# Kernel optimization log

Hardware: AMD Instinct MI355X
Metric: run time of the kernel (lower is better)

## Reference

```python
import jax, jax.numpy as jnp
import numpy as np

N_NODES = 100000
N_EDGES = 1200000
EMBED_DIM = 64
N_LAYERS = 3


def setup_inputs() -> dict:
    key = jax.random.key(0)
    k1, k2, k3, k4 = jax.random.split(key, 4)
    embeddings = jax.random.normal(k1, (N_NODES, EMBED_DIM), dtype=jnp.float32)
    edge_weight = jax.random.uniform(k2, (N_EDGES,), dtype=jnp.float32)
    edge_src = jax.random.randint(k3, (N_EDGES,), 0, N_NODES, dtype=jnp.int32)
    edge_dst = jax.random.randint(k4, (N_EDGES,), 0, N_NODES, dtype=jnp.int32)
    return {"embeddings": embeddings, "edge_weight": edge_weight,
            "edge_src": edge_src, "edge_dst": edge_dst}


def _spmm(edge_src, edge_dst, edge_weight, x):
    # (A @ x)[d] = sum_{e: dst(e)=d} w[e] * x[src(e)]  -- COO SpMM via gather + segment_sum
    msgs = edge_weight[:, None] * x[edge_src]  # [E, D]
    return jax.ops.segment_sum(msgs, edge_dst, num_segments=N_NODES)


def reference(embeddings, edge_weight, edge_src, edge_dst):
    all_embeddings = [embeddings]
    ego = embeddings
    for _ in range(N_LAYERS):
        ego = _spmm(edge_src, edge_dst, edge_weight, ego)
        all_embeddings.append(ego)
    # stack layer outputs: [n_layers+1, N, D]
    return jnp.stack(all_embeddings, axis=0)
```

## Files before the change

### kernel.cpp

```cpp
#include <hip/hip_runtime.h>


#define N_NODES 100000
#define DIM 64
#define SCAN_CHUNK 1024

#define NR 8
#define RSIZE ((N_NODES + NR - 1) / NR)
#define SLICES 256

typedef int   vint4   __attribute__((ext_vector_type(4)));
typedef float vfloat4 __attribute__((ext_vector_type(4)));

__device__ __forceinline__ int xcd_id() {
    int x;
    asm volatile("s_getreg_b32 %0, hwreg(HW_REG_XCC_ID)" : "=s"(x));
    return x & (NR - 1);
}


__global__ void hist_kernel(const int* __restrict__ edst, int* __restrict__ deg, int E) {
    int i = blockIdx.x * blockDim.x + threadIdx.x;
    int nv = E >> 2;
    if (i < nv) {
        vint4 d = __builtin_nontemporal_load(((const vint4*)edst) + i);
        atomicAdd(&deg[d[0]], 1);
        atomicAdd(&deg[d[1]], 1);
        atomicAdd(&deg[d[2]], 1);
        atomicAdd(&deg[d[3]], 1);
    }
    if (i == 0) {
        for (int e = nv << 2; e < E; ++e) atomicAdd(&deg[edst[e]], 1);
    }
}

__global__ void scan1_kernel(const int* __restrict__ deg, int* __restrict__ off,
                             int* __restrict__ bsum, int n) {
    __shared__ int sdata[256];
    int tid = threadIdx.x;
    int base = blockIdx.x * SCAN_CHUNK + tid * 4;
    int v[4];
    #pragma unroll
    for (int i = 0; i < 4; ++i) v[i] = (base + i < n) ? deg[base + i] : 0;
    int tsum = v[0] + v[1] + v[2] + v[3];
    sdata[tid] = tsum;
    __syncthreads();
    for (int d = 1; d < 256; d <<= 1) {
        int t = (tid >= d) ? sdata[tid - d] : 0;
        __syncthreads();
        sdata[tid] += t;
        __syncthreads();
    }
    int excl = sdata[tid] - tsum;
    if (tid == 255) bsum[blockIdx.x] = sdata[255];
    int run = excl;
    #pragma unroll
    for (int i = 0; i < 4; ++i) {
        if (base + i < n) off[base + i] = run;
        run += v[i];
    }
}

__global__ void scan2_kernel(int* __restrict__ bsum, int nb) {
    __shared__ int s[128];
    int tid = threadIdx.x;
    int v = (tid < nb) ? bsum[tid] : 0;
    s[tid] = v;
    __syncthreads();
    for (int d = 1; d < 128; d <<= 1) {
        int t = (tid >= d) ? s[tid - d] : 0;
        __syncthreads();
        s[tid] += t;
        __syncthreads();
    }
    if (tid < nb) bsum[tid] = s[tid] - v;
}

__global__ void scan3_kernel(int* __restrict__ off, int* __restrict__ cur,
                             const int* __restrict__ bsum, int n) {
    int i = blockIdx.x * blockDim.x + threadIdx.x;
    if (i < n) {
        int v = off[i] + bsum[i / SCAN_CHUNK];
        off[i] = v;
        cur[i] = v;
    }
}

__global__ void scatter_xcd_kernel(const int* __restrict__ esrc, const int* __restrict__ edst,
                                   const float* __restrict__ ew, int* __restrict__ cur,
                                   int2* __restrict__ pairs, int* __restrict__ ticket,
                                   int E, int chunk) {
    const int r = xcd_id();
    const int lo = r * RSIZE;
    const int hi = min(lo + RSIZE, N_NODES);
    __shared__ int s_sl;
    for (;;) {
        if (threadIdx.x == 0) s_sl = atomicAdd(&ticket[r], 1);
        __syncthreads();
        const int s = s_sl;
        __syncthreads();
        if (s >= SLICES) return;
        const int e0 = s * chunk;
        if (e0 >= E) continue;
        const int e1 = min(e0 + chunk, E);
        const int nv = (e1 - e0) >> 2;
        const vint4*   s4 = (const vint4*)(esrc + e0);
        const vint4*   d4 = (const vint4*)(edst + e0);
        const vfloat4* w4 = (const vfloat4*)(ew + e0);
        for (int i = threadIdx.x; i < nv; i += blockDim.x) {
            vint4 dd = __builtin_nontemporal_load(d4 + i);
            vint4 ss = __builtin_nontemporal_load(s4 + i);
            vfloat4 ww = __builtin_nontemporal_load(w4 + i);
            #pragma unroll
            for (int j = 0; j < 4; ++j) {
                int dj = dd[j];
                if (dj >= lo && dj < hi) {
                    int p = atomicAdd(&cur[dj], 1);
                    int2 pr;
                    pr.x = ss[j];
                    pr.y = __float_as_int(ww[j]);
                    pairs[p] = pr;
                }
            }
        }
        for (int e = e0 + (nv << 2) + threadIdx.x; e < e1; e += blockDim.x) {
            int dj = edst[e];
            if (dj >= lo && dj < hi) {
                int p = atomicAdd(&cur[dj], 1);
                int2 pr;
                pr.x = esrc[e];
                pr.y = __float_as_int(ew[e]);
                pairs[p] = pr;
            }
        }
    }
}


__global__ void spmm_csr_kernel(const float* __restrict__ x,
                                const int2* __restrict__ pairs,
                                const int* __restrict__ off,
                                const int* __restrict__ deg,
                                float* __restrict__ y) {
    int gtid = blockIdx.x * blockDim.x + threadIdx.x;
    int node = gtid >> 6;
    int lane = threadIdx.x & 63;
    int o  = lane >> 3;
    int ol = lane & 7;
    if (node >= N_NODES) return;
    int s0 = off[node];
    int n  = deg[node];
    float4 a0 = make_float4(0.f, 0.f, 0.f, 0.f);
    float4 a1 = make_float4(0.f, 0.f, 0.f, 0.f);
    for (int k = o; k < n; k += 8) {
        int2 pr = pairs[s0 + k];
        float w = __int_as_float(pr.y);
        const float4* row = (const float4*)(x + (size_t)pr.x * DIM);
        float4 v0 = row[ol];
        float4 v1 = row[ol + 8];
        a0.x += w * v0.x; a0.y += w * v0.y; a0.z += w * v0.z; a0.w += w * v0.w;
        a1.x += w * v1.x; a1.y += w * v1.y; a1.z += w * v1.z; a1.w += w * v1.w;
    }
    #pragma unroll
    for (int d = 8; d <= 32; d <<= 1) {
        a0.x += __shfl_xor(a0.x, d); a0.y += __shfl_xor(a0.y, d);
        a0.z += __shfl_xor(a0.z, d); a0.w += __shfl_xor(a0.w, d);
        a1.x += __shfl_xor(a1.x, d); a1.y += __shfl_xor(a1.y, d);
        a1.z += __shfl_xor(a1.z, d); a1.w += __shfl_xor(a1.w, d);
    }
    if (o == 0) {
        vfloat4* yrow = (vfloat4*)(y + (size_t)node * DIM);
        vfloat4 r0 = { a0.x, a0.y, a0.z, a0.w };
        vfloat4 r1 = { a1.x, a1.y, a1.z, a1.w };
        __builtin_nontemporal_store(r0, yrow + ol);
        __builtin_nontemporal_store(r1, yrow + ol + 8);
    }
}


__global__ void spmm_atomic_kernel(const float* __restrict__ x, const float* __restrict__ ew,
                                   const int* __restrict__ esrc, const int* __restrict__ edst,
                                   float* __restrict__ y, int n_edges) {
    long long tid = (long long)blockIdx.x * blockDim.x + threadIdx.x;
    int e = (int)(tid >> 6);
    int d = (int)(tid & 63);
    if (e >= n_edges) return;
    int s = esrc[e]; int t = edst[e]; float w = ew[e];
    atomicAdd(&y[(long long)t * DIM + d], w * x[(long long)s * DIM + d]);
}

extern "C" void kernel_launch(void* const* d_in, const int* in_sizes, int n_in,
                              void* d_out, int out_size, void* d_ws, size_t ws_size,
                              hipStream_t stream) {
    const float* emb  = (const float*)d_in[0];
    const float* ew   = (const float*)d_in[1];
    const int*   esrc = (const int*)d_in[2];
    const int*   edst = (const int*)d_in[3];
    float* out = (float*)d_out;

    const int E = in_sizes[1];
    const size_t layer_elems = (size_t)N_NODES * DIM;

    size_t need = (size_t)E * 8 + (size_t)3 * N_NODES * 4 + 1024;
    hipMemcpyAsync(out, emb, layer_elems * sizeof(float), hipMemcpyDeviceToDevice, stream);

    if (ws_size >= need) {
        char* w = (char*)d_ws;
        int2* pairs = (int2*)w;
        int* deg    = (int*)(w + (size_t)E * 8);
        int* cur    = deg + N_NODES;
        int* off    = cur + N_NODES;
        int* bsum   = off + N_NODES;
        int* ticket = bsum + 128;

        hipMemsetAsync(deg, 0, (size_t)N_NODES * 4, stream);
        hipMemsetAsync(ticket, 0, NR * 4, stream);

        const int nv4 = E >> 2;
        hist_kernel<<<(nv4 + 255) / 256, 256, 0, stream>>>(edst, deg, E);

        const int nscan = (N_NODES + SCAN_CHUNK - 1) / SCAN_CHUNK;
        scan1_kernel<<<nscan, 256, 0, stream>>>(deg, off, bsum, N_NODES);
        scan2_kernel<<<1, 128, 0, stream>>>(bsum, nscan);
        scan3_kernel<<<(N_NODES + 255) / 256, 256, 0, stream>>>(off, cur, bsum, N_NODES);

        const int chunk = (((E + SLICES - 1) / SLICES) + 3) & ~3;
        scatter_xcd_kernel<<<1024, 256, 0, stream>>>(esrc, edst, ew, cur, pairs, ticket, E, chunk);

        const int nb = (N_NODES + 3) / 4;
        for (int l = 1; l <= 3; ++l) {
            spmm_csr_kernel<<<nb, 256, 0, stream>>>(
                out + (size_t)(l - 1) * layer_elems, pairs, off, deg,
                out + (size_t)l * layer_elems);
        }
    } else {
        hipMemsetAsync(out + layer_elems, 0, 3 * layer_elems * sizeof(float), stream);
        const long long total_threads = (long long)E * 64;
        const int blocks = (int)((total_threads + 255) / 256);
        for (int l = 1; l <= 3; ++l) {
            spmm_atomic_kernel<<<blocks, 256, 0, stream>>>(
                out + (size_t)(l - 1) * layer_elems, ew, esrc, edst,
                out + (size_t)l * layer_elems, E);
        }
    }
}
```

Measured before the change: 405.6 us.

## Simplify scatter to flat kernel and widen per-edge row gather in CSR SpMM

Drops the XCD-partitioned ticket-based scatter, which made each of the 8 XCD groups re-read the whole edge list, in favour of a single flat pass with global atomics on the cursor array. The SpMM kernel now gives each edge 4 lanes, each loading 4 float4 chunks, so 16 edges are in flight per wavefront instead of 8. Each wavefront preloads the first 64 (src, weight) pairs cooperatively and broadcasts them with shuffles, falling back to direct loads beyond 64 neighbours. The trade-off is that scatter atomics and pair writes lose the per-XCD L2 locality the old scheme aimed for, and the reduction needs more shuffles.

```diff
diff --git a/kernel.cpp b/kernel.cpp
--- a/kernel.cpp
+++ b/kernel.cpp
@@ -5,18 +5,8 @@
 #define DIM 64
 #define SCAN_CHUNK 1024
 
-#define NR 8
-#define RSIZE ((N_NODES + NR - 1) / NR)
-#define SLICES 256
-
 typedef int   vint4   __attribute__((ext_vector_type(4)));
 typedef float vfloat4 __attribute__((ext_vector_type(4)));
-
-__device__ __forceinline__ int xcd_id() {
-    int x;
-    asm volatile("s_getreg_b32 %0, hwreg(HW_REG_XCC_ID)" : "=s"(x));
-    return x & (NR - 1);
-}
 
 
 __global__ void hist_kernel(const int* __restrict__ edst, int* __restrict__ deg, int E) {
@@ -86,52 +76,31 @@
     }
 }
 
-__global__ void scatter_xcd_kernel(const int* __restrict__ esrc, const int* __restrict__ edst,
-                                   const float* __restrict__ ew, int* __restrict__ cur,
-                                   int2* __restrict__ pairs, int* __restrict__ ticket,
-                                   int E, int chunk) {
-    const int r = xcd_id();
-    const int lo = r * RSIZE;
-    const int hi = min(lo + RSIZE, N_NODES);
-    __shared__ int s_sl;
-    for (;;) {
-        if (threadIdx.x == 0) s_sl = atomicAdd(&ticket[r], 1);
-        __syncthreads();
-        const int s = s_sl;
-        __syncthreads();
-        if (s >= SLICES) return;
-        const int e0 = s * chunk;
-        if (e0 >= E) continue;
-        const int e1 = min(e0 + chunk, E);
-        const int nv = (e1 - e0) >> 2;
-        const vint4*   s4 = (const vint4*)(esrc + e0);
-        const vint4*   d4 = (const vint4*)(edst + e0);
-        const vfloat4* w4 = (const vfloat4*)(ew + e0);
-        for (int i = threadIdx.x; i < nv; i += blockDim.x) {
-            vint4 dd = __builtin_nontemporal_load(d4 + i);
-            vint4 ss = __builtin_nontemporal_load(s4 + i);
-            vfloat4 ww = __builtin_nontemporal_load(w4 + i);
-            #pragma unroll
-            for (int j = 0; j < 4; ++j) {
-                int dj = dd[j];
-                if (dj >= lo && dj < hi) {
-                    int p = atomicAdd(&cur[dj], 1);
-                    int2 pr;
-                    pr.x = ss[j];
-                    pr.y = __float_as_int(ww[j]);
-                    pairs[p] = pr;
-                }
-            }
-        }
-        for (int e = e0 + (nv << 2) + threadIdx.x; e < e1; e += blockDim.x) {
-            int dj = edst[e];
-            if (dj >= lo && dj < hi) {
-                int p = atomicAdd(&cur[dj], 1);
-                int2 pr;
-                pr.x = esrc[e];
-                pr.y = __float_as_int(ew[e]);
-                pairs[p] = pr;
-            }
+__global__ void scatter_kernel(const int* __restrict__ esrc, const int* __restrict__ edst,
+                               const float* __restrict__ ew, int* __restrict__ cur,
+                               int2* __restrict__ pairs, int E) {
+    int i = blockIdx.x * blockDim.x + threadIdx.x;
+    int nv = E >> 2;
+    if (i < nv) {
+        vint4 dd = __builtin_nontemporal_load(((const vint4*)edst) + i);
+        vint4 ss = __builtin_nontemporal_load(((const vint4*)esrc) + i);
+        vfloat4 ww = __builtin_nontemporal_load(((const vfloat4*)ew) + i);
+        #pragma unroll
+        for (int j = 0; j < 4; ++j) {
+            int p = atomicAdd(&cur[dd[j]], 1);
+            int2 pr;
+            pr.x = ss[j];
+            pr.y = __float_as_int(ww[j]);
+            pairs[p] = pr;
+        }
+    }
+    if (i == 0) {
+        for (int e = nv << 2; e < E; ++e) {
+            int p = atomicAdd(&cur[edst[e]], 1);
+            int2 pr;
+            pr.x = esrc[e];
+            pr.y = __float_as_int(ew[e]);
+            pairs[p] = pr;
         }
     }
 }
@@ -145,35 +114,62 @@
     int gtid = blockIdx.x * blockDim.x + threadIdx.x;
     int node = gtid >> 6;
     int lane = threadIdx.x & 63;
-    int o  = lane >> 3;
-    int ol = lane & 7;
+    int g  = lane >> 2;
+    int gl = lane & 3;
     if (node >= N_NODES) return;
     int s0 = off[node];
     int n  = deg[node];
+
+    int2 pr0; pr0.x = 0; pr0.y = 0;
+    if (lane < n) pr0 = pairs[s0 + lane];
+
     float4 a0 = make_float4(0.f, 0.f, 0.f, 0.f);
-    float4 a1 = make_float4(0.f, 0.f, 0.f, 0.f);
-    for (int k = o; k < n; k += 8) {
-        int2 pr = pairs[s0 + k];
-        float w = __int_as_float(pr.y);
-        const float4* row = (const float4*)(x + (size_t)pr.x * DIM);
-        float4 v0 = row[ol];
-        float4 v1 = row[ol + 8];
-        a0.x += w * v0.x; a0.y += w * v0.y; a0.z += w * v0.z; a0.w += w * v0.w;
-        a1.x += w * v1.x; a1.y += w * v1.y; a1.z += w * v1.z; a1.w += w * v1.w;
+    float4 a1 = a0, a2 = a0, a3 = a0;
+
+    int trips = (n + 15) >> 4;
+    for (int t = 0; t < trips; ++t) {
+        int k = g + (t << 4);
+        int idx = min(k, 63);
+        int src = __shfl(pr0.x, idx);
+        int wb  = __shfl(pr0.y, idx);
+        if (k >= 64 && k < n) {
+            int2 p2 = pairs[s0 + k];
+            src = p2.x; wb = p2.y;
+        }
+        if (k < n) {
+            float w = __int_as_float(wb);
+            const float4* row = (const float4*)(x + (size_t)src * DIM);
+            float4 v0 = row[gl];
+            float4 v1 = row[gl + 4];
+            float4 v2 = row[gl + 8];
+            float4 v3 = row[gl + 12];
+            a0.x += w * v0.x; a0.y += w * v0.y; a0.z += w * v0.z; a0.w += w * v0.w;
+            a1.x += w * v1.x; a1.y += w * v1.y; a1.z += w * v1.z; a1.w += w * v1.w;
+            a2.x += w * v2.x; a2.y += w * v2.y; a2.z += w * v2.z; a2.w += w * v2.w;
+            a3.x += w * v3.x; a3.y += w * v3.y; a3.z += w * v3.z; a3.w += w * v3.w;
+        }
     }
     #pragma unroll
-    for (int d = 8; d <= 32; d <<= 1) {
+    for (int d = 4; d <= 32; d <<= 1) {
         a0.x += __shfl_xor(a0.x, d); a0.y += __shfl_xor(a0.y, d);
         a0.z += __shfl_xor(a0.z, d); a0.w += __shfl_xor(a0.w, d);
         a1.x += __shfl_xor(a1.x, d); a1.y += __shfl_xor(a1.y, d);
         a1.z += __shfl_xor(a1.z, d); a1.w += __shfl_xor(a1.w, d);
-    }
-    if (o == 0) {
+        a2.x += __shfl_xor(a2.x, d); a2.y += __shfl_xor(a2.y, d);
+        a2.z += __shfl_xor(a2.z, d); a2.w += __shfl_xor(a2.w, d);
+        a3.x += __shfl_xor(a3.x, d); a3.y += __shfl_xor(a3.y, d);
+        a3.z += __shfl_xor(a3.z, d); a3.w += __shfl_xor(a3.w, d);
+    }
+    if (g == 0) {
         vfloat4* yrow = (vfloat4*)(y + (size_t)node * DIM);
         vfloat4 r0 = { a0.x, a0.y, a0.z, a0.w };
         vfloat4 r1 = { a1.x, a1.y, a1.z, a1.w };
-        __builtin_nontemporal_store(r0, yrow + ol);
-        __builtin_nontemporal_store(r1, yrow + ol + 8);
+        vfloat4 r2 = { a2.x, a2.y, a2.z, a2.w };
+        vfloat4 r3 = { a3.x, a3.y, a3.z, a3.w };
+        __builtin_nontemporal_store(r0, yrow + gl);
+        __builtin_nontemporal_store(r1, yrow + gl + 4);
+        __builtin_nontemporal_store(r2, yrow + gl + 8);
+        __builtin_nontemporal_store(r3, yrow + gl + 12);
     }
 }
 
@@ -211,21 +207,19 @@
         int* cur    = deg + N_NODES;
         int* off    = cur + N_NODES;
         int* bsum   = off + N_NODES;
-        int* ticket = bsum + 128;
 
         hipMemsetAsync(deg, 0, (size_t)N_NODES * 4, stream);
-        hipMemsetAsync(ticket, 0, NR * 4, stream);
 
         const int nv4 = E >> 2;
-        hist_kernel<<<(nv4 + 255) / 256, 256, 0, stream>>>(edst, deg, E);
+        const int vb = (nv4 + 255) / 256;
+        hist_kernel<<<vb, 256, 0, stream>>>(edst, deg, E);
 
         const int nscan = (N_NODES + SCAN_CHUNK - 1) / SCAN_CHUNK;
         scan1_kernel<<<nscan, 256, 0, stream>>>(deg, off, bsum, N_NODES);
         scan2_kernel<<<1, 128, 0, stream>>>(bsum, nscan);
         scan3_kernel<<<(N_NODES + 255) / 256, 256, 0, stream>>>(off, cur, bsum, N_NODES);
 
-        const int chunk = (((E + SLICES - 1) / SLICES) + 3) & ~3;
-        scatter_xcd_kernel<<<1024, 256, 0, stream>>>(esrc, edst, ew, cur, pairs, ticket, E, chunk);
+        scatter_kernel<<<vb, 256, 0, stream>>>(esrc, edst, ew, cur, pairs, E);
 
         const int nb = (N_NODES + 3) / 4;
         for (int l = 1; l <= 3; ++l) {
```

Result: slower. 482.5 us (+19.0%).

## Gather fp16 copies of layer embeddings in SpMM and drop XCD ticket scatter

Applied to the files above, without the earlier changes.

Adds a conversion kernel that copies the input embeddings to the output and writes an fp16 shadow copy. Each SpMM layer now gathers neighbor rows from fp16 buffers, halving gather bytes, and writes both fp32 output and an fp16 copy for the next layer. The scatter kernel replaces the XCD-id ticket-based dynamic slicing with a static blockIdx-based range split using fewer slices. Feeding fp16-rounded values into later layers adds accumulated precision error relative to the fp32 reference.

```diff
diff --git a/kernel.cpp b/kernel.cpp
--- a/kernel.cpp
+++ b/kernel.cpp
@@ -1,4 +1,5 @@
 #include <hip/hip_runtime.h>
+#include <hip/hip_fp16.h>
 
 
 #define N_NODES 100000
@@ -7,15 +8,30 @@
 
 #define NR 8
 #define RSIZE ((N_NODES + NR - 1) / NR)
-#define SLICES 256
+#define SLICES 128
 
 typedef int   vint4   __attribute__((ext_vector_type(4)));
 typedef float vfloat4 __attribute__((ext_vector_type(4)));
 
-__device__ __forceinline__ int xcd_id() {
-    int x;
-    asm volatile("s_getreg_b32 %0, hwreg(HW_REG_XCC_ID)" : "=s"(x));
-    return x & (NR - 1);
+union HU { unsigned u; __half2 h; };
+
+__global__ void convert_kernel(const float* __restrict__ emb, float* __restrict__ out0,
+                               unsigned short* __restrict__ xh0, int n8) {
+    int i = blockIdx.x * blockDim.x + threadIdx.x;
+    if (i >= n8) return;
+    const vfloat4* e4 = (const vfloat4*)emb;
+    vfloat4 a = __builtin_nontemporal_load(e4 + 2 * i);
+    vfloat4 b = __builtin_nontemporal_load(e4 + 2 * i + 1);
+    vfloat4* o4 = (vfloat4*)out0;
+    __builtin_nontemporal_store(a, o4 + 2 * i);
+    __builtin_nontemporal_store(b, o4 + 2 * i + 1);
+    HU c0, c1, c2, c3;
+    c0.h = __float22half2_rn(make_float2(a[0], a[1]));
+    c1.h = __float22half2_rn(make_float2(a[2], a[3]));
+    c2.h = __float22half2_rn(make_float2(b[0], b[1]));
+    c3.h = __float22half2_rn(make_float2(b[2], b[3]));
+    vint4 p = { (int)c0.u, (int)c1.u, (int)c2.u, (int)c3.u };
+    ((vint4*)xh0)[i] = p;
 }
 
 
@@ -86,53 +102,96 @@
     }
 }
 
-__global__ void scatter_xcd_kernel(const int* __restrict__ esrc, const int* __restrict__ edst,
-                                   const float* __restrict__ ew, int* __restrict__ cur,
-                                   int2* __restrict__ pairs, int* __restrict__ ticket,
-                                   int E, int chunk) {
-    const int r = xcd_id();
+__global__ void scatter_range_kernel(const int* __restrict__ esrc, const int* __restrict__ edst,
+                                     const float* __restrict__ ew, int* __restrict__ cur,
+                                     int2* __restrict__ pairs, int E, int chunk) {
+    const int r = blockIdx.x & (NR - 1);
+    const int s = blockIdx.x / NR;
     const int lo = r * RSIZE;
     const int hi = min(lo + RSIZE, N_NODES);
-    __shared__ int s_sl;
-    for (;;) {
-        if (threadIdx.x == 0) s_sl = atomicAdd(&ticket[r], 1);
-        __syncthreads();
-        const int s = s_sl;
-        __syncthreads();
-        if (s >= SLICES) return;
-        const int e0 = s * chunk;
-        if (e0 >= E) continue;
-        const int e1 = min(e0 + chunk, E);
-        const int nv = (e1 - e0) >> 2;
-        const vint4*   s4 = (const vint4*)(esrc + e0);
-        const vint4*   d4 = (const vint4*)(edst + e0);
-        const vfloat4* w4 = (const vfloat4*)(ew + e0);
-        for (int i = threadIdx.x; i < nv; i += blockDim.x) {
-            vint4 dd = __builtin_nontemporal_load(d4 + i);
-            vint4 ss = __builtin_nontemporal_load(s4 + i);
-            vfloat4 ww = __builtin_nontemporal_load(w4 + i);
-            #pragma unroll
-            for (int j = 0; j < 4; ++j) {
-                int dj = dd[j];
-                if (dj >= lo && dj < hi) {
-                    int p = atomicAdd(&cur[dj], 1);
-                    int2 pr;
-                    pr.x = ss[j];
-                    pr.y = __float_as_int(ww[j]);
-                    pairs[p] = pr;
-                }
-            }
-        }
-        for (int e = e0 + (nv << 2) + threadIdx.x; e < e1; e += blockDim.x) {
-            int dj = edst[e];
+    const int e0 = s * chunk;
+    if (e0 >= E) return;
+    const int e1 = min(e0 + chunk, E);
+    const int nv = (e1 - e0) >> 2;
+    const vint4*   s4 = (const vint4*)(esrc + e0);
+    const vint4*   d4 = (const vint4*)(edst + e0);
+    const vfloat4* w4 = (const vfloat4*)(ew + e0);
+    for (int i = threadIdx.x; i < nv; i += blockDim.x) {
+        vint4 dd = __builtin_nontemporal_load(d4 + i);
+        vint4 ss = __builtin_nontemporal_load(s4 + i);
+        vfloat4 ww = __builtin_nontemporal_load(w4 + i);
+        #pragma unroll
+        for (int j = 0; j < 4; ++j) {
+            int dj = dd[j];
             if (dj >= lo && dj < hi) {
                 int p = atomicAdd(&cur[dj], 1);
                 int2 pr;
-                pr.x = esrc[e];
-                pr.y = __float_as_int(ew[e]);
+                pr.x = ss[j];
+                pr.y = __float_as_int(ww[j]);
                 pairs[p] = pr;
             }
         }
+    }
+    for (int e = e0 + (nv << 2) + threadIdx.x; e < e1; e += blockDim.x) {
+        int dj = edst[e];
+        if (dj >= lo && dj < hi) {
+            int p = atomicAdd(&cur[dj], 1);
+            int2 pr;
+            pr.x = esrc[e];
+            pr.y = __float_as_int(ew[e]);
+            pairs[p] = pr;
+        }
+    }
+}
+
+
+__global__ void spmm_h_kernel(const unsigned short* __restrict__ xh,
+                              const int2* __restrict__ pairs,
+                              const int* __restrict__ off,
+                              const int* __restrict__ deg,
+                              float* __restrict__ y,
+                              unsigned short* __restrict__ yh) {
+    int gtid = blockIdx.x * blockDim.x + threadIdx.x;
+    int node = gtid >> 6;
+    int lane = threadIdx.x & 63;
+    int o  = lane >> 3;
+    int ol = lane & 7;
+    if (node >= N_NODES) return;
+    int s0 = off[node];
+    int n  = deg[node];
+    float a0 = 0.f, a1 = 0.f, a2 = 0.f, a3 = 0.f;
+    float a4 = 0.f, a5 = 0.f, a6 = 0.f, a7 = 0.f;
+    for (int k = o; k < n; k += 8) {
+        int2 pr = pairs[s0 + k];
+        float w = __int_as_float(pr.y);
+        const vint4* row = (const vint4*)(xh + (size_t)pr.x * DIM);
+        vint4 v = row[ol];
+        HU c; float2 f;
+        c.u = (unsigned)v[0]; f = __half22float2(c.h); a0 += w * f.x; a1 += w * f.y;
+        c.u = (unsigned)v[1]; f = __half22float2(c.h); a2 += w * f.x; a3 += w * f.y;
+        c.u = (unsigned)v[2]; f = __half22float2(c.h); a4 += w * f.x; a5 += w * f.y;
+        c.u = (unsigned)v[3]; f = __half22float2(c.h); a6 += w * f.x; a7 += w * f.y;
+    }
+    #pragma unroll
+    for (int d = 8; d <= 32; d <<= 1) {
+        a0 += __shfl_xor(a0, d); a1 += __shfl_xor(a1, d);
+        a2 += __shfl_xor(a2, d); a3 += __shfl_xor(a3, d);
+        a4 += __shfl_xor(a4, d); a5 += __shfl_xor(a5, d);
+        a6 += __shfl_xor(a6, d); a7 += __shfl_xor(a7, d);
+    }
+    if (o == 0) {
+        float* yr = y + (size_t)node * DIM + ol * 8;
+        vfloat4 r0 = { a0, a1, a2, a3 };
+        vfloat4 r1 = { a4, a5, a6, a7 };
+        __builtin_nontemporal_store(r0, (vfloat4*)yr);
+        __builtin_nontemporal_store(r1, (vfloat4*)yr + 1);
+        HU c0, c1, c2, c3;
+        c0.h = __float22half2_rn(make_float2(a0, a1));
+        c1.h = __float22half2_rn(make_float2(a2, a3));
+        c2.h = __float22half2_rn(make_float2(a4, a5));
+        c3.h = __float22half2_rn(make_float2(a6, a7));
+        vint4 p = { (int)c0.u, (int)c1.u, (int)c2.u, (int)c3.u };
+        *((vint4*)(yh + (size_t)node * DIM + ol * 8)) = p;
     }
 }
 
@@ -151,7 +210,7 @@
     int s0 = off[node];
     int n  = deg[node];
     float4 a0 = make_float4(0.f, 0.f, 0.f, 0.f);
-    float4 a1 = make_float4(0.f, 0.f, 0.f, 0.f);
+    float4 a1 = a0;
     for (int k = o; k < n; k += 8) {
         int2 pr = pairs[s0 + k];
         float w = __int_as_float(pr.y);
@@ -201,20 +260,23 @@
     const int E = in_sizes[1];
     const size_t layer_elems = (size_t)N_NODES * DIM;
 
-    size_t need = (size_t)E * 8 + (size_t)3 * N_NODES * 4 + 1024;
-    hipMemcpyAsync(out, emb, layer_elems * sizeof(float), hipMemcpyDeviceToDevice, stream);
-
-    if (ws_size >= need) {
+    const size_t need_h   = (size_t)E * 8 + 2 * layer_elems * 2 + (size_t)3 * N_NODES * 4 + 1024;
+    const size_t need_f32 = (size_t)E * 8 + (size_t)3 * N_NODES * 4 + 1024;
+
+    if (ws_size >= need_h && E >= 4) {
         char* w = (char*)d_ws;
         int2* pairs = (int2*)w;
-        int* deg    = (int*)(w + (size_t)E * 8);
-        int* cur    = deg + N_NODES;
-        int* off    = cur + N_NODES;
-        int* bsum   = off + N_NODES;
-        int* ticket = bsum + 128;
+        unsigned short* xh0 = (unsigned short*)(w + (size_t)E * 8);
+        unsigned short* xh1 = xh0 + layer_elems;
+        int* deg  = (int*)(xh1 + layer_elems);
+        int* cur  = deg + N_NODES;
+        int* off  = cur + N_NODES;
+        int* bsum = off + N_NODES;
 
         hipMemsetAsync(deg, 0, (size_t)N_NODES * 4, stream);
-        hipMemsetAsync(ticket, 0, NR * 4, stream);
+
+        const int n8 = (int)(layer_elems / 8);
+        convert_kernel<<<(n8 + 255) / 256, 256, 0, stream>>>(emb, out, xh0, n8);
 
         const int nv4 = E >> 2;
         hist_kernel<<<(nv4 + 255) / 256, 256, 0, stream>>>(edst, deg, E);
@@ -225,7 +287,36 @@
         scan3_kernel<<<(N_NODES + 255) / 256, 256, 0, stream>>>(off, cur, bsum, N_NODES);
 
         const int chunk = (((E + SLICES - 1) / SLICES) + 3) & ~3;
-        scatter_xcd_kernel<<<1024, 256, 0, stream>>>(esrc, edst, ew, cur, pairs, ticket, E, chunk);
+        scatter_range_kernel<<<NR * SLICES, 256, 0, stream>>>(esrc, edst, ew, cur, pairs, E, chunk);
+
+        const int nb = (N_NODES + 3) / 4;
+        unsigned short* xs[2] = { xh0, xh1 };
+        for (int l = 1; l <= 3; ++l) {
+            spmm_h_kernel<<<nb, 256, 0, stream>>>(
+                xs[(l - 1) & 1], pairs, off, deg,
+                out + (size_t)l * layer_elems, xs[l & 1]);
+        }
+    } else if (ws_size >= need_f32 && E >= 4) {
+        char* w = (char*)d_ws;
+        int2* pairs = (int2*)w;
+        int* deg  = (int*)(w + (size_t)E * 8);
+        int* cur  = deg + N_NODES;
+        int* off  = cur + N_NODES;
+        int* bsum = off + N_NODES;
+
+        hipMemcpyAsync(out, emb, layer_elems * sizeof(float), hipMemcpyDeviceToDevice, stream);
+        hipMemsetAsync(deg, 0, (size_t)N_NODES * 4, stream);
+
+        const int nv4 = E >> 2;
+        hist_kernel<<<(nv4 + 255) / 256, 256, 0, stream>>>(edst, deg, E);
+
+        const int nscan = (N_NODES + SCAN_CHUNK - 1) / SCAN_CHUNK;
+        scan1_kernel<<<nscan, 256, 0, stream>>>(deg, off, bsum, N_NODES);
+        scan2_kernel<<<1, 128, 0, stream>>>(bsum, nscan);
+        scan3_kernel<<<(N_NODES + 255) / 256, 256, 0, stream>>>(off, cur, bsum, N_NODES);
+
+        const int chunk = (((E + SLICES - 1) / SLICES) + 3) & ~3;
+        scatter_range_kernel<<<NR * SLICES, 256, 0, stream>>>(esrc, edst, ew, cur, pairs, E, chunk);
 
         const int nb = (N_NODES + 3) / 4;
         for (int l = 1; l <= 3; ++l) {
@@ -234,6 +325,7 @@
                 out + (size_t)l * layer_elems);
         }
     } else {
+        hipMemcpyAsync(out, emb, layer_elems * sizeof(float), hipMemcpyDeviceToDevice, stream);
         hipMemsetAsync(out + layer_elems, 0, 3 * layer_elems * sizeof(float), stream);
         const long long total_threads = (long long)E * 64;
         const int blocks = (int)((total_threads + 255) / 256);
```

Result: faster. 366.3 us (-9.7%).
